# Performance work log

Hardware: AMD Instinct MI355X
Metric: run time of the kernel (lower is better)

The kernel has to match this reference:

```python
import jax, jax.numpy as jnp
import numpy as np

K = 4
N_UP = 50
N_DOWN = 50


def setup_inputs() -> dict:
    key = jax.random.key(0)
    k1, k2, k3, k4 = jax.random.split(key, 4)
    B, N, D = 2048, 100, 128
    configs = jax.random.randint(k1, (B, N), 0, 4, dtype=jnp.int64)
    tok_table = jax.random.normal(k2, (4, D), dtype=jnp.float32)
    pos_table = jax.random.normal(k3, (144, D), dtype=jnp.float32)
    W_orb = jax.random.normal(k4, (K * (N_UP + N_DOWN), D), dtype=jnp.float32) * 0.01
    b_orb = jnp.zeros((K * (N_UP + N_DOWN),), dtype=jnp.float32)
    return {"configs": configs, "tok_table": tok_table, "pos_table": pos_table,
            "W_orb": W_orb, "b_orb": b_orb}


def _occ_idx(mask, n_occ):
    # indices of occupied sites first (stable argsort of -mask), then sorted ascending
    idx = jnp.argsort(-mask.astype(jnp.float32), axis=1)[:, :n_occ]
    return jnp.sort(idx, axis=1)


def reference(configs, tok_table, pos_table, W_orb, b_orb):
    B, N = configs.shape
    # encode_input + identity backbone
    h = tok_table[configs] + pos_table[jnp.arange(N)][None, :, :]  # (B,N,D)
    orb = jnp.einsum('bnd,od->bno', h, W_orb) + b_orb               # (B,N,K*(nu+nd))
    orb_up = orb[..., :K * N_UP].reshape(B, N, K, N_UP).transpose(0, 2, 1, 3)
    orb_dn = orb[..., K * N_UP:].reshape(B, N, K, N_DOWN).transpose(0, 2, 1, 3)
    has_up = (configs == 1) | (configs == 3)
    has_dn = (configs == 2) | (configs == 3)
    up_idx = _occ_idx(has_up, N_UP)      # (B,n_up)
    dn_idx = _occ_idx(has_dn, N_DOWN)    # (B,n_down)
    phi_up = jnp.take_along_axis(orb_up, up_idx[:, None, :, None], axis=2)  # (B,K,nu,nu)
    phi_dn = jnp.take_along_axis(orb_dn, dn_idx[:, None, :, None], axis=2)  # (B,K,nd,nd)
    det_up = jnp.linalg.det(phi_up)  # (B,K)
    det_dn = jnp.linalg.det(phi_dn)  # (B,K)
    psi = jnp.sum(det_up * det_dn, axis=1)  # (B,)
    log_abs = jnp.log(jnp.abs(psi) + 1e-30)
    phase = jnp.where(psi >= 0, 0.0, jnp.pi).astype(jnp.float32)
    return jax.lax.complex(log_abs.astype(jnp.float32), phase)
```

## Files before the change

### kernel.cpp

```cpp
#include <hip/hip_runtime.h>
#include <math.h>

#define NSITE 100
#define NOCC  50
#define DIM   128
#define KDET  4
#define NTAB  400
#define TP_FLOATS ((4 + 144) * NTAB)


__device__ __forceinline__ unsigned dpp_max64_to_lane63(unsigned x) {
  unsigned t;
  t = (unsigned)__builtin_amdgcn_update_dpp((int)x, (int)x, 0x111, 0xf, 0xf, false);
  x = x > t ? x : t;
  t = (unsigned)__builtin_amdgcn_update_dpp((int)x, (int)x, 0x112, 0xf, 0xf, false);
  x = x > t ? x : t;
  t = (unsigned)__builtin_amdgcn_update_dpp((int)x, (int)x, 0x114, 0xf, 0xf, false);
  x = x > t ? x : t;
  t = (unsigned)__builtin_amdgcn_update_dpp((int)x, (int)x, 0x118, 0xf, 0xf, false);
  x = x > t ? x : t;
  t = (unsigned)__builtin_amdgcn_update_dpp((int)x, (int)x, 0x142, 0xa, 0xf, false);
  x = x > t ? x : t;
  t = (unsigned)__builtin_amdgcn_update_dpp((int)x, (int)x, 0x143, 0xc, 0xf, false);
  x = x > t ? x : t;
  return x;
}

#define REPC(X) X(0) X(1) X(2) X(3) X(4) X(5) X(6) X(7) X(8) X(9) \
  X(10) X(11) X(12) X(13) X(14) X(15) X(16) X(17) X(18) X(19) \
  X(20) X(21) X(22) X(23) X(24)

__global__ __launch_bounds__(256) void tp_kernel(
    const float* __restrict__ tok, const float* __restrict__ pos,
    const float* __restrict__ W,   const float* __restrict__ bvec,
    float* __restrict__ T, float* __restrict__ P)
{
  const int gid = blockIdx.x * 256 + threadIdx.x;
  if (gid >= 148 * NTAB) return;
  const int row = gid / NTAB;
  const int col = gid - row * NTAB;
  const float4* h4 = (const float4*)((row < 4) ? (tok + (size_t)row * DIM)
                                               : (pos + (size_t)(row - 4) * DIM));
  const float4* w4 = (const float4*)(W + (size_t)col * DIM);
  float acc = 0.0f;
  #pragma unroll
  for (int i = 0; i < DIM / 4; ++i) {
    float4 a = h4[i], b = w4[i];
    acc = fmaf(a.x, b.x, acc);
    acc = fmaf(a.y, b.y, acc);
    acc = fmaf(a.z, b.z, acc);
    acc = fmaf(a.w, b.w, acc);
  }
  if (row < 4) T[(size_t)row * NTAB + col] = acc;
  else         P[(size_t)(row - 4) * NTAB + col] = acc + bvec[col];
}

__global__ __launch_bounds__(256)
__attribute__((amdgpu_waves_per_eu(8)))
void det_kernel(
    const int*   __restrict__ configs,
    const float* __restrict__ T,
    const float* __restrict__ P,
    double*      __restrict__ dets)
{
  const int b    = blockIdx.x;
  const int spin = blockIdx.y;

  __shared__ unsigned long long omask[2];
  __shared__ float stash[4][25][50];
  __shared__ unsigned char cfg8[NSITE];
  __shared__ unsigned char idx8[NOCC];

  const int tid = threadIdx.x;

  bool occv = false;
  if (tid < NSITE) {
    const int c = configs[(size_t)b * NSITE + tid];
    cfg8[tid] = (unsigned char)c;
    occv = (spin == 0) ? (c == 1 || c == 3) : (c == 2 || c == 3);
  }
  const unsigned long long bal = __ballot(occv);
  if ((tid & 63) == 0 && tid < 128) omask[tid >> 6] = bal;
  __syncthreads();
  if (tid < NSITE) {
    const unsigned long long m0 = omask[0], m1 = omask[1];
    const int mtot = __popcll(m0) + __popcll(m1);
    const int need = (mtot < NOCC) ? (NOCC - mtot) : 0;
    int pocc;
    if (tid >= 64) pocc = __popcll(m0) + __popcll(m1 & ((1ull << (tid - 64)) - 1ull));
    else           pocc = __popcll(m0 & ((1ull << tid) - 1ull));
    const int punocc = tid - pocc;
    const bool sel = occv ? (pocc < NOCC) : (punocc < need);
    const int  poscap = (pocc  < NOCC) ? pocc  : NOCC;
    const int  pfill  = (punocc < need) ? punocc : need;
    if (sel) idx8[poscap + pfill] = (unsigned char)tid;
  }
  __syncthreads();

  const int lane = tid & 63;
  const int wave = tid >> 6;
  const int wave_u  = __builtin_amdgcn_readfirstlane(wave);
  const int colbase = spin * 200 + wave_u * 50;

  const bool act  = (lane < NOCC);
  const int  site = idx8[act ? lane : 0];
  const int  cc0  = cfg8[site];
  const float* Trow = T + (size_t)cc0  * NTAB + colbase;
  const float* Prow = P + (size_t)site * NTAB + colbase;
  const float2* T2 = (const float2*)Trow;
  const float2* P2 = (const float2*)Prow;

  #define DECLC(i) float c##i;
  REPC(DECLC)
  #undef DECLC
  #define LQ(i0, i1) { float2 a = T2[(i0) / 2], d = P2[(i0) / 2]; \
      c##i0 = a.x + d.x; c##i1 = a.y + d.y; }
  LQ(0, 1)  LQ(2, 3)  LQ(4, 5)  LQ(6, 7)  LQ(8, 9)  LQ(10, 11)
  LQ(12, 13) LQ(14, 15) LQ(16, 17) LQ(18, 19) LQ(20, 21) LQ(22, 23)
  #undef LQ
  c24 = Trow[24] + Prow[24];
  #define ZC(i) c##i = act ? c##i : 0.0f;
  REPC(ZC)
  #undef ZC

  unsigned aliveq = act ? 0xFFFFFFFFu : 0u;
  float    mant_prod = 1.0f;
  int      esum = 0;
  unsigned sgnx = 0u;
  unsigned long long chosen = 0ull;
  int      invsum = 0;
  const unsigned lu = (unsigned)lane;
  unsigned long long pp[3] = {0ull, 0ull, 0ull};

  #define UC(L) { const float pc = __int_as_float( \
      __builtin_amdgcn_readlane(__float_as_int(c##L), p)); \
      c##L = fmaf(-mult, pc, c##L); }
  #define UCF_25
  #define UCF_24 UC(24)
  #define UCF_23 UC(23) UCF_24
  #define UCF_22 UC(22) UCF_23
  #define UCF_21 UC(21) UCF_22
  #define UCF_20 UC(20) UCF_21
  #define UCF_19 UC(19) UCF_20
  #define UCF_18 UC(18) UCF_19
  #define UCF_17 UC(17) UCF_18
  #define UCF_16 UC(16) UCF_17
  #define UCF_15 UC(15) UCF_16
  #define UCF_14 UC(14) UCF_15
  #define UCF_13 UC(13) UCF_14
  #define UCF_12 UC(12) UCF_13
  #define UCF_11 UC(11) UCF_12
  #define UCF_10 UC(10) UCF_11
  #define UCF_9  UC(9)  UCF_10
  #define UCF_8  UC(8)  UCF_9
  #define UCF_7  UC(7)  UCF_8
  #define UCF_6  UC(6)  UCF_7
  #define UCF_5  UC(5)  UCF_6
  #define UCF_4  UC(4)  UCF_5
  #define UCF_3  UC(3)  UCF_4
  #define UCF_2  UC(2)  UCF_3
  #define UCF_1  UC(1)  UCF_2

  #define P1STEP(J, N) { \
    unsigned key = ((__float_as_uint(c##J) & 0x7FFFFFC0u) | lu) & aliveq; \
    key = dpp_max64_to_lane63(key); \
    const int p = __builtin_amdgcn_readlane((int)key, 63) & 63; \
    const unsigned pb = (unsigned)__builtin_amdgcn_readlane( \
        __float_as_int(c##J), p); \
    esum += (int)((pb >> 23) & 0xFFu) - 127; \
    sgnx ^= (pb & 0x80000000u); \
    mant_prod *= __uint_as_float((pb & 0x007FFFFFu) | 0x3F800000u); \
    invsum += __popcll(chosen >> (p + 1)); \
    chosen |= 1ull << (unsigned)p; \
    aliveq = (lane == p) ? 0u : aliveq; \
    pp[(J) / 10] |= ((unsigned long long)(unsigned)p) << (6 * ((J) % 10)); \
    const float piv = __uint_as_float(pb); \
    float r0 = __builtin_amdgcn_rcpf(piv); \
    r0 = fmaf(fmaf(-piv, r0, 1.0f), r0, r0); \
    const float rp = ((pb & 0x7FFFFFFFu) != 0u) ? r0 : 0.0f; \
    const float mult = __uint_as_float(__float_as_uint(c##J * rp) & aliveq); \
    if (act) stash[wave_u][(J)][lane] = mult; \
    UCF_##N \
  }

  P1STEP(0,1)   P1STEP(1,2)   P1STEP(2,3)   P1STEP(3,4)   P1STEP(4,5)
  P1STEP(5,6)   P1STEP(6,7)   P1STEP(7,8)   P1STEP(8,9)   P1STEP(9,10)
  P1STEP(10,11) P1STEP(11,12) P1STEP(12,13) P1STEP(13,14) P1STEP(14,15)
  P1STEP(15,16) P1STEP(16,17) P1STEP(17,18) P1STEP(18,19) P1STEP(19,20)
  P1STEP(20,21) P1STEP(21,22) P1STEP(22,23) P1STEP(23,24) P1STEP(24,25)
  #undef P1STEP

  #define DECLT(i) float t##i;
  REPC(DECLT)
  #undef DECLT
  #define LT(i) t##i = Trow[25 + (i)] + Prow[25 + (i)];
  REPC(LT)
  #undef LT
  #define ZT(i) t##i = act ? t##i : 0.0f;
  REPC(ZT)
  #undef ZT

  #define BT(L) { const float pc = __int_as_float( \
      __builtin_amdgcn_ds_bpermute(pa, __float_as_int(t##L))); \
      t##L = fmaf(-mult, pc, t##L); }

  #define P2J(J) { \
    const int pa = ((int)((pp[(J) / 10] >> (6 * ((J) % 10))) & 63ull)) << 2; \
    const float mult = stash[wave_u][(J)][lane < NOCC ? lane : 0]; \
    BT(0)  BT(1)  BT(2)  BT(3)  BT(4)  BT(5) \
    __builtin_amdgcn_sched_barrier(0); \
    BT(6)  BT(7)  BT(8)  BT(9)  BT(10) BT(11) \
    __builtin_amdgcn_sched_barrier(0); \
    BT(12) BT(13) BT(14) BT(15) BT(16) BT(17) \
    __builtin_amdgcn_sched_barrier(0); \
    BT(18) BT(19) BT(20) BT(21) BT(22) BT(23) BT(24) \
    __builtin_amdgcn_sched_barrier(0); \
  }
  P2J(0)  P2J(1)  P2J(2)  P2J(3)  P2J(4)  P2J(5)  P2J(6)  P2J(7)
  P2J(8)  P2J(9)  P2J(10) P2J(11) P2J(12) P2J(13) P2J(14) P2J(15)
  P2J(16) P2J(17) P2J(18) P2J(19) P2J(20) P2J(21) P2J(22) P2J(23)
  P2J(24)
  #undef P2J
  #undef BT

  #define UT(L) { const float pc = __int_as_float( \
      __builtin_amdgcn_readlane(__float_as_int(t##L), p)); \
      t##L = fmaf(-mult, pc, t##L); }
  #define UTF_25
  #define UTF_24 UT(24)
  #define UTF_23 UT(23) UTF_24
  #define UTF_22 UT(22) UTF_23
  #define UTF_21 UT(21) UTF_22
  #define UTF_20 UT(20) UTF_21
  #define UTF_19 UT(19) UTF_20
  #define UTF_18 UT(18) UTF_19
  #define UTF_17 UT(17) UTF_18
  #define UTF_16 UT(16) UTF_17
  #define UTF_15 UT(15) UTF_16
  #define UTF_14 UT(14) UTF_15
  #define UTF_13 UT(13) UTF_14
  #define UTF_12 UT(12) UTF_13
  #define UTF_11 UT(11) UTF_12
  #define UTF_10 UT(10) UTF_11
  #define UTF_9  UT(9)  UTF_10
  #define UTF_8  UT(8)  UTF_9
  #define UTF_7  UT(7)  UTF_8
  #define UTF_6  UT(6)  UTF_7
  #define UTF_5  UT(5)  UTF_6
  #define UTF_4  UT(4)  UTF_5
  #define UTF_3  UT(3)  UTF_4
  #define UTF_2  UT(2)  UTF_3
  #define UTF_1  UT(1)  UTF_2

  #define P3STEP(L, N) { \
    unsigned key = ((__float_as_uint(t##L) & 0x7FFFFFC0u) | lu) & aliveq; \
    key = dpp_max64_to_lane63(key); \
    const int p = __builtin_amdgcn_readlane((int)key, 63) & 63; \
    const unsigned pb = (unsigned)__builtin_amdgcn_readlane( \
        __float_as_int(t##L), p); \
    esum += (int)((pb >> 23) & 0xFFu) - 127; \
    sgnx ^= (pb & 0x80000000u); \
    mant_prod *= __uint_as_float((pb & 0x007FFFFFu) | 0x3F800000u); \
    invsum += __popcll(chosen >> (p + 1)); \
    chosen |= 1ull << (unsigned)p; \
    aliveq = (lane == p) ? 0u : aliveq; \
    const float piv = __uint_as_float(pb); \
    float r0 = __builtin_amdgcn_rcpf(piv); \
    r0 = fmaf(fmaf(-piv, r0, 1.0f), r0, r0); \
    const float rp = ((pb & 0x7FFFFFFFu) != 0u) ? r0 : 0.0f; \
    const float mult = __uint_as_float(__float_as_uint(t##L * rp) & aliveq); \
    UTF_##N \
  }

  P3STEP(0,1)   P3STEP(1,2)   P3STEP(2,3)   P3STEP(3,4)   P3STEP(4,5)
  P3STEP(5,6)   P3STEP(6,7)   P3STEP(7,8)   P3STEP(8,9)   P3STEP(9,10)
  P3STEP(10,11) P3STEP(11,12) P3STEP(12,13) P3STEP(13,14) P3STEP(14,15)
  P3STEP(15,16) P3STEP(16,17) P3STEP(17,18) P3STEP(18,19) P3STEP(19,20)
  P3STEP(20,21) P3STEP(21,22) P3STEP(22,23) P3STEP(23,24) P3STEP(24,25)
  #undef P3STEP
  #undef UT
  #undef UC

  const double logdet =
      log((double)mant_prod) + (double)esum * 0.6931471805599453;
  const int sgn = (((sgnx >> 31) + (unsigned)invsum) & 1u) ? -1 : 1;

  if (lane == 0) {
    size_t o = (((size_t)b * 2 + spin) * KDET + wave) * 2;
    dets[o]     = logdet;
    dets[o + 1] = (double)sgn;
  }
}

__global__ __launch_bounds__(256) void combine_kernel(
    const double* __restrict__ dets, float* __restrict__ out, int B)
{
  int b = blockIdx.x * blockDim.x + threadIdx.x;
  if (b >= B) return;
  const double* du = dets + ((size_t)b * 2 + 0) * KDET * 2;
  const double* dd = dets + ((size_t)b * 2 + 1) * KDET * 2;
  double t[KDET], s[KDET], m = -1e300;
  #pragma unroll
  for (int k = 0; k < KDET; ++k) {
    t[k] = du[2 * k] + dd[2 * k];
    s[k] = du[2 * k + 1] * dd[2 * k + 1];
    if (t[k] > m) m = t[k];
  }
  double sum = 0.0;
  #pragma unroll
  for (int k = 0; k < KDET; ++k) {
    if (t[k] > -1e290) sum += s[k] * exp(t[k] - m);
  }
  double p  = (m > -1e290) ? exp(m) * fabs(sum) : 0.0;
  double la = log(p + 1e-30);
  float phase = (sum >= 0.0) ? 0.0f : 3.14159265358979f;
  out[b]     = (float)la;
  out[B + b] = phase;
}

extern "C" void kernel_launch(void* const* d_in, const int* in_sizes, int n_in,
                              void* d_out, int out_size, void* d_ws, size_t ws_size,
                              hipStream_t stream) {
  const int*   configs = (const int*)  d_in[0];
  const float* tok     = (const float*)d_in[1];
  const float* pos     = (const float*)d_in[2];
  const float* W       = (const float*)d_in[3];
  const float* bv      = (const float*)d_in[4];

  float*  wsf  = (float*)d_ws;
  float*  T    = wsf;
  float*  P    = wsf + 4 * NTAB;
  double* dets = (double*)(wsf + TP_FLOATS);
  const int B = in_sizes[0] / NSITE;

  tp_kernel<<<(148 * NTAB + 255) / 256, 256, 0, stream>>>(tok, pos, W, bv, T, P);
  dim3 grid(B, 2);
  det_kernel<<<grid, 256, 0, stream>>>(configs, T, P, dets);
  combine_kernel<<<(B + 255) / 256, 256, 0, stream>>>(dets, (float*)d_out, B);
}
```

Measured before the change: 195.7 us.

## Fuse both spins and combine step into one det block; split tp dot product

Each det block now handles both spin channels with 8 waves (512 threads) and does the final log-sum-exp combine in shared memory, so the combine kernel launch and the global dets buffer round-trip go away. The table-precompute kernel splits each 128-length dot product across 4 lanes and reduces them with shuffles, which gives it more parallelism. The costs are higher per-block shared memory (stash doubled) and a 512-thread launch bound that may lower occupancy or raise register pressure. The extra block-wide barrier before the combine also serializes the spins.

```diff
diff --git a/kernel.cpp b/kernel.cpp
--- a/kernel.cpp
+++ b/kernel.cpp
@@ -36,75 +36,94 @@
     float* __restrict__ T, float* __restrict__ P)
 {
   const int gid = blockIdx.x * 256 + threadIdx.x;
-  if (gid >= 148 * NTAB) return;
-  const int row = gid / NTAB;
-  const int col = gid - row * NTAB;
+  if (gid >= 148 * NTAB * 4) return;
+  const int q   = gid >> 2;
+  const int h   = gid & 3;
+  const int row = q / NTAB;
+  const int col = q - row * NTAB;
   const float4* h4 = (const float4*)((row < 4) ? (tok + (size_t)row * DIM)
                                                : (pos + (size_t)(row - 4) * DIM));
   const float4* w4 = (const float4*)(W + (size_t)col * DIM);
   float acc = 0.0f;
   #pragma unroll
-  for (int i = 0; i < DIM / 4; ++i) {
-    float4 a = h4[i], b = w4[i];
+  for (int i = 0; i < 8; ++i) {
+    float4 a = h4[h * 8 + i], b = w4[h * 8 + i];
     acc = fmaf(a.x, b.x, acc);
     acc = fmaf(a.y, b.y, acc);
     acc = fmaf(a.z, b.z, acc);
     acc = fmaf(a.w, b.w, acc);
   }
-  if (row < 4) T[(size_t)row * NTAB + col] = acc;
-  else         P[(size_t)(row - 4) * NTAB + col] = acc + bvec[col];
+  acc += __shfl_xor(acc, 1);
+  acc += __shfl_xor(acc, 2);
+  if (h == 0) {
+    if (row < 4) T[(size_t)row * NTAB + col] = acc;
+    else         P[(size_t)(row - 4) * NTAB + col] = acc + bvec[col];
+  }
 }
 
-__global__ __launch_bounds__(256)
+__global__ __launch_bounds__(512)
 __attribute__((amdgpu_waves_per_eu(8)))
 void det_kernel(
     const int*   __restrict__ configs,
     const float* __restrict__ T,
     const float* __restrict__ P,
-    double*      __restrict__ dets)
+    float*       __restrict__ out,
+    int B)
 {
-  const int b    = blockIdx.x;
-  const int spin = blockIdx.y;
-
-  __shared__ unsigned long long omask[2];
-  __shared__ float stash[4][25][50];
-  __shared__ unsigned char cfg8[NSITE];
-  __shared__ unsigned char idx8[NOCC];
+  const int b = blockIdx.x;
+
+  __shared__ float stash[8][25][50];
+  __shared__ int cfg[NSITE];
+  __shared__ int idxs[2][NOCC];
+  __shared__ unsigned long long omask[2][2];
+  __shared__ double detl[2][KDET][2];
 
   const int tid = threadIdx.x;
 
-  bool occv = false;
+  int  cval = 0;
+  bool ou = false, od = false;
   if (tid < NSITE) {
-    const int c = configs[(size_t)b * NSITE + tid];
-    cfg8[tid] = (unsigned char)c;
-    occv = (spin == 0) ? (c == 1 || c == 3) : (c == 2 || c == 3);
-  }
-  const unsigned long long bal = __ballot(occv);
-  if ((tid & 63) == 0 && tid < 128) omask[tid >> 6] = bal;
+    cval = configs[(size_t)b * NSITE + tid];
+    cfg[tid] = cval;
+    ou = (cval == 1) || (cval == 3);
+    od = (cval == 2) || (cval == 3);
+  }
+  const unsigned long long balu = __ballot(ou);
+  const unsigned long long bald = __ballot(od);
+  if ((tid & 63) == 0 && tid < 128) {
+    omask[0][tid >> 6] = balu;
+    omask[1][tid >> 6] = bald;
+  }
   __syncthreads();
   if (tid < NSITE) {
-    const unsigned long long m0 = omask[0], m1 = omask[1];
-    const int mtot = __popcll(m0) + __popcll(m1);
-    const int need = (mtot < NOCC) ? (NOCC - mtot) : 0;
-    int pocc;
-    if (tid >= 64) pocc = __popcll(m0) + __popcll(m1 & ((1ull << (tid - 64)) - 1ull));
-    else           pocc = __popcll(m0 & ((1ull << tid) - 1ull));
-    const int punocc = tid - pocc;
-    const bool sel = occv ? (pocc < NOCC) : (punocc < need);
-    const int  poscap = (pocc  < NOCC) ? pocc  : NOCC;
-    const int  pfill  = (punocc < need) ? punocc : need;
-    if (sel) idx8[poscap + pfill] = (unsigned char)tid;
+    #pragma unroll
+    for (int s = 0; s < 2; ++s) {
+      const unsigned long long m0 = omask[s][0], m1 = omask[s][1];
+      const bool occv = (s == 0) ? ou : od;
+      const int mtot = __popcll(m0) + __popcll(m1);
+      const int need = (mtot < NOCC) ? (NOCC - mtot) : 0;
+      int pocc;
+      if (tid >= 64) pocc = __popcll(m0) + __popcll(m1 & ((1ull << (tid - 64)) - 1ull));
+      else           pocc = __popcll(m0 & ((1ull << tid) - 1ull));
+      const int punocc = tid - pocc;
+      const bool sel = occv ? (pocc < NOCC) : (punocc < need);
+      const int  poscap = (pocc  < NOCC) ? pocc  : NOCC;
+      const int  pfill  = (punocc < need) ? punocc : need;
+      if (sel) idxs[s][poscap + pfill] = tid;
+    }
   }
   __syncthreads();
 
-  const int lane = tid & 63;
-  const int wave = tid >> 6;
-  const int wave_u  = __builtin_amdgcn_readfirstlane(wave);
-  const int colbase = spin * 200 + wave_u * 50;
+  const int lane   = tid & 63;
+  const int wave   = tid >> 6;
+  const int wave_u = __builtin_amdgcn_readfirstlane(wave);
+  const int spin   = wave_u >> 2;
+  const int kd     = wave_u & 3;
+  const int colbase = spin * 200 + kd * 50;
 
   const bool act  = (lane < NOCC);
-  const int  site = idx8[act ? lane : 0];
-  const int  cc0  = cfg8[site];
+  const int  site = idxs[spin][act ? lane : 0];
+  const int  cc0  = cfg[site];
   const float* Trow = T + (size_t)cc0  * NTAB + colbase;
   const float* Prow = P + (size_t)site * NTAB + colbase;
   const float2* T2 = (const float2*)Trow;
@@ -286,36 +305,29 @@
   const int sgn = (((sgnx >> 31) + (unsigned)invsum) & 1u) ? -1 : 1;
 
   if (lane == 0) {
-    size_t o = (((size_t)b * 2 + spin) * KDET + wave) * 2;
-    dets[o]     = logdet;
-    dets[o + 1] = (double)sgn;
-  }
-}
-
-__global__ __launch_bounds__(256) void combine_kernel(
-    const double* __restrict__ dets, float* __restrict__ out, int B)
-{
-  int b = blockIdx.x * blockDim.x + threadIdx.x;
-  if (b >= B) return;
-  const double* du = dets + ((size_t)b * 2 + 0) * KDET * 2;
-  const double* dd = dets + ((size_t)b * 2 + 1) * KDET * 2;
-  double t[KDET], s[KDET], m = -1e300;
-  #pragma unroll
-  for (int k = 0; k < KDET; ++k) {
-    t[k] = du[2 * k] + dd[2 * k];
-    s[k] = du[2 * k + 1] * dd[2 * k + 1];
-    if (t[k] > m) m = t[k];
-  }
-  double sum = 0.0;
-  #pragma unroll
-  for (int k = 0; k < KDET; ++k) {
-    if (t[k] > -1e290) sum += s[k] * exp(t[k] - m);
-  }
-  double p  = (m > -1e290) ? exp(m) * fabs(sum) : 0.0;
-  double la = log(p + 1e-30);
-  float phase = (sum >= 0.0) ? 0.0f : 3.14159265358979f;
-  out[b]     = (float)la;
-  out[B + b] = phase;
+    detl[spin][kd][0] = logdet;
+    detl[spin][kd][1] = (double)sgn;
+  }
+  __syncthreads();
+
+  if (tid == 0) {
+    double t[KDET], s[KDET], m = -1e300;
+    #pragma unroll
+    for (int k2 = 0; k2 < KDET; ++k2) {
+      t[k2] = detl[0][k2][0] + detl[1][k2][0];
+      s[k2] = detl[0][k2][1] * detl[1][k2][1];
+      if (t[k2] > m) m = t[k2];
+    }
+    double sum = 0.0;
+    #pragma unroll
+    for (int k2 = 0; k2 < KDET; ++k2) {
+      if (t[k2] > -1e290) sum += s[k2] * exp(t[k2] - m);
+    }
+    double pw = (m > -1e290) ? exp(m) * fabs(sum) : 0.0;
+    double la = log(pw + 1e-30);
+    out[b]     = (float)la;
+    out[B + b] = (sum >= 0.0) ? 0.0f : 3.14159265358979f;
+  }
 }
 
 extern "C" void kernel_launch(void* const* d_in, const int* in_sizes, int n_in,
@@ -330,11 +342,8 @@
   float*  wsf  = (float*)d_ws;
   float*  T    = wsf;
   float*  P    = wsf + 4 * NTAB;
-  double* dets = (double*)(wsf + TP_FLOATS);
   const int B = in_sizes[0] / NSITE;
 
-  tp_kernel<<<(148 * NTAB + 255) / 256, 256, 0, stream>>>(tok, pos, W, bv, T, P);
-  dim3 grid(B, 2);
-  det_kernel<<<grid, 256, 0, stream>>>(configs, T, P, dets);
-  combine_kernel<<<(B + 255) / 256, 256, 0, stream>>>(dets, (float*)d_out, B);
+  tp_kernel<<<(148 * NTAB * 4 + 255) / 256, 256, 0, stream>>>(tok, pos, W, bv, T, P);
+  det_kernel<<<B, 512, 0, stream>>>(configs, T, P, (float*)d_out, B);
 }
```

Result: no change. 195.2 us (-0.3%).
